# Kernel optimization log

Hardware: AMD Instinct MI355X
Metric: run time of the kernel (lower is better)

## Reference

```python
import jax, jax.numpy as jnp
import numpy as np

D_MODEL = 1024
N_HEAD = 16


def setup_inputs() -> dict:
    key = jax.random.key(0)
    ks = jax.random.split(key, 11)
    B, S, D = 2, 2048, D_MODEL
    scale = 1.0 / np.sqrt(D)
    inp = {
        "q": jax.random.normal(ks[0], (B, S, D), jnp.float32),
        "k": jax.random.normal(ks[1], (B, S, D), jnp.float32),
        "v": jax.random.normal(ks[2], (B, S, D), jnp.float32),
        "w_q": jax.random.normal(ks[3], (D, D), jnp.float32) * scale,
        "b_q": jnp.zeros((D,), jnp.float32),
        "w_k": jax.random.normal(ks[4], (D, D), jnp.float32) * scale,
        "b_k": jnp.zeros((D,), jnp.float32),
        "w_v": jax.random.normal(ks[5], (D, D), jnp.float32) * scale,
        "b_v": jnp.zeros((D,), jnp.float32),
        "w_o": jax.random.normal(ks[6], (D, D), jnp.float32) * scale,
        "b_o": jnp.zeros((D,), jnp.float32),
    }
    return inp


def _split_heads(x, n_head):
    # [B, S, D] -> [B, H, S, Dh]
    B, S, D = x.shape
    return x.reshape(B, S, n_head, D // n_head).transpose(0, 2, 1, 3)


def reference(q, k, v, w_q, b_q, w_k, b_k, w_v, b_v, w_o, b_o):
    # torch Linear: y = x @ W.T + b
    qp = q @ w_q.T + b_q
    kp = k @ w_k.T + b_k
    vp = v @ w_v.T + b_v
    qh = _split_heads(qp, N_HEAD)  # [B,H,S,Dh]
    kh = _split_heads(kp, N_HEAD)
    vh = _split_heads(vp, N_HEAD)
    d_head = qh.shape[-1]
    score = jnp.einsum("bhsd,bhtd->bhst", qh, kh) / jnp.sqrt(jnp.float32(d_head))
    attn = jax.nn.softmax(score, axis=-1)
    out = jnp.einsum("bhst,bhtd->bhsd", attn, vh)  # [B,H,S,Dh]
    B, H, S, Dh = out.shape
    out = out.transpose(0, 2, 1, 3).reshape(B, S, H * Dh)  # concat heads
    return out @ w_o.T + b_o
```

## Files before the change

kernel.cpp:

```cpp
#include <hip/hip_runtime.h>

typedef __bf16 bf16_t;
typedef __bf16 bf16x8 __attribute__((ext_vector_type(8)));
typedef __bf16 bf16x4 __attribute__((ext_vector_type(4)));
typedef float f32x4 __attribute__((ext_vector_type(4)));

#define MFMA16(a, b, c) __builtin_amdgcn_mfma_f32_16x16x32_bf16((a), (b), (c), 0, 0, 0)

#define GLOAD_LDS16(gsrc, ldst)                                                     \
  __builtin_amdgcn_global_load_lds(                                                 \
      (const __attribute__((address_space(1))) void*)(gsrc),                        \
      (__attribute__((address_space(3))) void*)(ldst), 16, 0, 0)

__global__ __launch_bounds__(256) void cast_all(
    const float* __restrict__ s0, const float* __restrict__ s1, const float* __restrict__ s2,
    const float* __restrict__ s3, const float* __restrict__ s4, const float* __restrict__ s5,
    const float* __restrict__ s6,
    bf16_t* __restrict__ d0, bf16_t* __restrict__ d1, bf16_t* __restrict__ d2,
    bf16_t* __restrict__ d3, bf16_t* __restrict__ d4, bf16_t* __restrict__ d5,
    bf16_t* __restrict__ d6) {
  const int a = blockIdx.y;
  const float* s = a == 0 ? s0 : a == 1 ? s1 : a == 2 ? s2 : a == 3 ? s3
                 : a == 4 ? s4 : a == 5 ? s5 : s6;
  bf16_t* d = a == 0 ? d0 : a == 1 ? d1 : a == 2 ? d2 : a == 3 ? d3
            : a == 4 ? d4 : a == 5 ? d5 : d6;
  const int n = a < 3 ? (2 * 2048 * 1024) : (1024 * 1024);
  int i = (blockIdx.x * 256 + threadIdx.x) * 4;
  if (i >= n) return;
  float4 v = *reinterpret_cast<const float4*>(s + i);
  bf16x4 o;
  o[0] = (bf16_t)v.x; o[1] = (bf16_t)v.y; o[2] = (bf16_t)v.z; o[3] = (bf16_t)v.w;
  *reinterpret_cast<bf16x4*>(d + i) = o;
}

template <int OUTF32>
__device__ __forceinline__ void gemm_core(
    const bf16_t* __restrict__ A, const bf16_t* __restrict__ B,
    const float* __restrict__ bias, void* __restrict__ Cout,
    int bm, int bn, float scalep, bf16_t* __restrict__ As, bf16_t* __restrict__ Bs) {
  const int tid = threadIdx.x, lane = tid & 63, wid = tid >> 6;
  const int wr = wid >> 1, wc = wid & 1;
  const int l15 = lane & 15, g = lane >> 4, l7 = l15 & 7;
  const int sr = lane >> 3;
  const int sg = (lane & 7) ^ sr;
  f32x4 acc[4][2] = {};

  const bf16_t* Arow = A + (size_t)(bm + wid * 32 + sr) * 1024 + sg * 8;
  const bf16_t* Brow = B + (size_t)(bn + wid * 16 + sr) * 1024 + sg * 8;

  auto stage = [&](int t, int buf) {
    const int k0 = t * 64;
    bf16_t* Ad = As + buf * 8192 + wid * 2048;
    bf16_t* Bd = Bs + buf * 4096 + wid * 1024;
#pragma unroll
    for (int a = 0; a < 4; a++)
      GLOAD_LDS16(Arow + (size_t)a * 8 * 1024 + k0, Ad + a * 512);
#pragma unroll
    for (int bI = 0; bI < 2; bI++)
      GLOAD_LDS16(Brow + (size_t)bI * 8 * 1024 + k0, Bd + bI * 512);
  };

  stage(0, 0);
  __syncthreads();
  for (int t = 0; t < 16; t++) {
    if (t < 15) stage(t + 1, (t + 1) & 1);
    const bf16_t* Ab = As + (t & 1) * 8192;
    const bf16_t* Bb = Bs + (t & 1) * 4096;
#pragma unroll
    for (int kk = 0; kk < 2; kk++) {
      const int gsw = ((kk * 4 + g) ^ l7) * 8;
      bf16x8 af[4], bfr[2];
#pragma unroll
      for (int mi = 0; mi < 4; mi++)
        af[mi] = *reinterpret_cast<const bf16x8*>(&Ab[(wr * 64 + mi * 16 + l15) * 64 + gsw]);
#pragma unroll
      for (int ni = 0; ni < 2; ni++)
        bfr[ni] = *reinterpret_cast<const bf16x8*>(&Bb[(wc * 32 + ni * 16 + l15) * 64 + gsw]);
      __builtin_amdgcn_s_setprio(1);
#pragma unroll
      for (int mi = 0; mi < 4; mi++)
#pragma unroll
        for (int ni = 0; ni < 2; ni++)
          acc[mi][ni] = MFMA16(af[mi], bfr[ni], acc[mi][ni]);
      __builtin_amdgcn_s_setprio(0);
    }
    __syncthreads();
  }

#pragma unroll
  for (int mi = 0; mi < 4; mi++)
#pragma unroll
    for (int ni = 0; ni < 2; ni++) {
      const int row = bm + wr * 64 + mi * 16 + g * 4;
      const int col = bn + wc * 32 + ni * 16 + l15;
      const float bv = bias[col];
#pragma unroll
      for (int r = 0; r < 4; r++) {
        float v = (acc[mi][ni][r] + bv) * scalep;
        if (OUTF32)
          reinterpret_cast<float*>(Cout)[(size_t)(row + r) * 1024 + col] = v;
        else
          reinterpret_cast<bf16_t*>(Cout)[(size_t)(row + r) * 1024 + col] = (bf16_t)v;
      }
    }
}

__global__ __launch_bounds__(256) void qkv_gemm(
    const bf16_t* __restrict__ qb, const bf16_t* __restrict__ kb, const bf16_t* __restrict__ vb,
    const bf16_t* __restrict__ wqb, const bf16_t* __restrict__ wkb, const bf16_t* __restrict__ wvb,
    const float* __restrict__ bq, const float* __restrict__ bk, const float* __restrict__ bv,
    bf16_t* __restrict__ QP, bf16_t* __restrict__ KP, bf16_t* __restrict__ VP, float qscale) {
  __shared__ bf16_t As[2 * 128 * 64];
  __shared__ bf16_t Bs[2 * 64 * 64];
  const int id = blockIdx.x;
  const int sw = (id & 7) * 192 + (id >> 3);
  const int z = sw >> 9, rem = sw & 511;
  const int by = rem >> 4, bx = rem & 15;
  const bf16_t* A = z == 0 ? qb : z == 1 ? kb : vb;
  const bf16_t* B = z == 0 ? wqb : z == 1 ? wkb : wvb;
  const float* bias = z == 0 ? bq : z == 1 ? bk : bv;
  bf16_t* C = z == 0 ? QP : z == 1 ? KP : VP;
  gemm_core<0>(A, B, bias, C, by * 128, bx * 64, z == 0 ? qscale : 1.0f, As, Bs);
}

__global__ __launch_bounds__(256) void out_gemm(
    const bf16_t* __restrict__ A, const bf16_t* __restrict__ B,
    const float* __restrict__ bias, float* __restrict__ C) {
  __shared__ bf16_t As[2 * 128 * 64];
  __shared__ bf16_t Bs[2 * 64 * 64];
  const int id = blockIdx.x;
  const int sw = (id & 7) * 64 + (id >> 3);
  const int by = sw >> 4, bx = sw & 15;
  gemm_core<1>(A, B, bias, C, by * 128, bx * 64, 1.0f, As, Bs);
}

__global__ __launch_bounds__(256) void transpose_v64(
    const bf16_t* __restrict__ VP, bf16_t* __restrict__ VT) {
  __shared__ bf16_t t[64][72];
  const int tid = threadIdx.x;
  const int bh = blockIdx.y, b = bh >> 4, h = bh & 15;
  const int sbase = blockIdx.x * 64;
#pragma unroll
  for (int i = 0; i < 2; i++) {
    int c = tid + i * 256;
    int r = c >> 3, cc = (c & 7) * 8;
    *reinterpret_cast<bf16x8*>(&t[r][cc]) =
        *reinterpret_cast<const bf16x8*>(&VP[(size_t)(b * 2048 + sbase + r) * 1024 + h * 64 + cc]);
  }
  __syncthreads();
#pragma unroll
  for (int i = 0; i < 2; i++) {
    int c = tid + i * 256;
    int d = c >> 3, scc = (c & 7) * 8;
    bf16x8 v;
#pragma unroll
    for (int j = 0; j < 8; j++) v[j] = t[scc + j][d];
    *reinterpret_cast<bf16x8*>(&VT[(size_t)(bh * 64 + d) * 2048 + sbase + scc]) = v;
  }
}

__global__ __launch_bounds__(512) void attn_fwd(
    const bf16_t* __restrict__ Q, const bf16_t* __restrict__ K,
    const bf16_t* __restrict__ VT, bf16_t* __restrict__ O) {
  __shared__ bf16_t Kl[2 * 64 * 64];
  __shared__ bf16_t Vl[2 * 64 * 64];
  __shared__ bf16_t Pl[8][16 * 64];
  const int tid = threadIdx.x, lane = tid & 63, wid = tid >> 6;
  const int l15 = lane & 15, g = lane >> 4, l7 = l15 & 7;
  const int id = blockIdx.x;
  const int sw = (id & 7) * 64 + (id >> 3);
  const int bh = sw >> 4, qblk = sw & 15;
  const int b = bh >> 4, h = bh & 15;
  const int qbase = qblk * 128;

  const int qrow = b * 2048 + qbase + wid * 16 + l15;
  const bf16x8 qf0 = *reinterpret_cast<const bf16x8*>(&Q[(size_t)qrow * 1024 + h * 64 + g * 8]);
  const bf16x8 qf1 = *reinterpret_cast<const bf16x8*>(&Q[(size_t)qrow * 1024 + h * 64 + 32 + g * 8]);

  const int sr = lane >> 3, sg = (lane & 7) ^ sr;
  const bf16_t* Ksrc = K + (size_t)(b * 2048 + wid * 8 + sr) * 1024 + h * 64 + sg * 8;
  const bf16_t* Vsrc = VT + (size_t)(bh * 64 + wid * 8 + sr) * 2048 + sg * 8;

  float ssum = 0.0f;
  f32x4 oacc[4] = {};

  auto stage = [&](int kt, int buf) {
    GLOAD_LDS16(Ksrc + (size_t)kt * 1024, Kl + buf * 4096 + wid * 512);
    GLOAD_LDS16(Vsrc + kt, Vl + buf * 4096 + wid * 512);
  };

  stage(0, 0);
  __syncthreads();
  for (int t = 0; t < 32; t++) {
    if (t < 31) stage((t + 1) * 64, (t + 1) & 1);
    const bf16_t* Kb = Kl + (t & 1) * 4096;
    const bf16_t* Vb = Vl + (t & 1) * 4096;

    f32x4 sacc[4] = {};
    __builtin_amdgcn_s_setprio(1);
#pragma unroll
    for (int ni = 0; ni < 4; ni++) {
      const int krow = (ni * 16 + l15) * 64;
      bf16x8 kf0 = *reinterpret_cast<const bf16x8*>(&Kb[krow + ((g ^ l7) * 8)]);
      bf16x8 kf1 = *reinterpret_cast<const bf16x8*>(&Kb[krow + (((4 + g) ^ l7) * 8)]);
      sacc[ni] = MFMA16(kf0, qf0, sacc[ni]);
      sacc[ni] = MFMA16(kf1, qf1, sacc[ni]);
    }
    __builtin_amdgcn_s_setprio(0);

    float rs = 0.0f;
#pragma unroll
    for (int ni = 0; ni < 4; ni++)
#pragma unroll
      for (int r = 0; r < 4; r++) {
        float e = exp2f(sacc[ni][r]);
        sacc[ni][r] = e;
        rs += e;
      }
    rs += __shfl_xor(rs, 16);
    rs += __shfl_xor(rs, 32);
    ssum += rs;

#pragma unroll
    for (int ni = 0; ni < 4; ni++) {
      bf16x4 pv;
#pragma unroll
      for (int r = 0; r < 4; r++) pv[r] = (bf16_t)sacc[ni][r];
      *reinterpret_cast<bf16x4*>(
          &Pl[wid][l15 * 64 + (((2 * ni + (g >> 1)) ^ l7) * 8) + (g & 1) * 4]) = pv;
    }

    __builtin_amdgcn_s_setprio(1);
#pragma unroll
    for (int c = 0; c < 2; c++) {
      const int gp = ((c * 4 + g) ^ l7) * 8;
      bf16x8 pf = *reinterpret_cast<const bf16x8*>(&Pl[wid][l15 * 64 + gp]);
#pragma unroll
      for (int dn = 0; dn < 4; dn++) {
        bf16x8 vf = *reinterpret_cast<const bf16x8*>(&Vb[(dn * 16 + l15) * 64 + gp]);
        oacc[dn] = MFMA16(pf, vf, oacc[dn]);
      }
    }
    __builtin_amdgcn_s_setprio(0);
    __syncthreads();
  }

  float si[4];
#pragma unroll
  for (int r = 0; r < 4; r++) si[r] = 1.0f / __shfl(ssum, g * 4 + r);
  const int orow = b * 2048 + qbase + wid * 16 + g * 4;
#pragma unroll
  for (int dn = 0; dn < 4; dn++)
#pragma unroll
    for (int r = 0; r < 4; r++)
      O[(size_t)(orow + r) * 1024 + h * 64 + dn * 16 + l15] = (bf16_t)(oacc[dn][r] * si[r]);
}

extern "C" void kernel_launch(void* const* d_in, const int* in_sizes, int n_in,
                              void* d_out, int out_size, void* d_ws, size_t ws_size,
                              hipStream_t stream) {
  const float* q  = (const float*)d_in[0];
  const float* k  = (const float*)d_in[1];
  const float* v  = (const float*)d_in[2];
  const float* wq = (const float*)d_in[3];
  const float* bq = (const float*)d_in[4];
  const float* wk = (const float*)d_in[5];
  const float* bk = (const float*)d_in[6];
  const float* wv = (const float*)d_in[7];
  const float* bv = (const float*)d_in[8];
  const float* wo = (const float*)d_in[9];
  const float* bo = (const float*)d_in[10];

  char* ws = (char*)d_ws;
  const size_t MB = 1024 * 1024;
  bf16_t* qb  = (bf16_t*)(ws + 0 * MB);
  bf16_t* kb  = (bf16_t*)(ws + 8 * MB);
  bf16_t* vb  = (bf16_t*)(ws + 16 * MB);
  bf16_t* QP  = (bf16_t*)(ws + 24 * MB);
  bf16_t* KP  = (bf16_t*)(ws + 32 * MB);
  bf16_t* VP  = (bf16_t*)(ws + 40 * MB);
  bf16_t* wqb = (bf16_t*)(ws + 48 * MB);
  bf16_t* wkb = (bf16_t*)(ws + 50 * MB);
  bf16_t* wvb = (bf16_t*)(ws + 52 * MB);
  bf16_t* wob = (bf16_t*)(ws + 54 * MB);
  bf16_t* VTb = (bf16_t*)(ws + 8 * MB);
  bf16_t* AO  = (bf16_t*)(ws + 0 * MB);

  const float QSCALE = 0.125f * 1.44269504089f;

  cast_all<<<dim3(4096, 7), 256, 0, stream>>>(q, k, v, wq, wk, wv, wo,
                                              qb, kb, vb, wqb, wkb, wvb, wob);
  qkv_gemm<<<1536, 256, 0, stream>>>(qb, kb, vb, wqb, wkb, wvb, bq, bk, bv,
                                     QP, KP, VP, QSCALE);
  transpose_v64<<<dim3(32, 32), 256, 0, stream>>>(VP, VTb);
  attn_fwd<<<512, 512, 0, stream>>>(QP, KP, VTb, AO);
  out_gemm<<<512, 256, 0, stream>>>(AO, wob, bo, (float*)d_out);
}
```

Baseline: 237.8 us.

## Enlarge GEMM tiles to 128x128 and move attention to 32x32 MFMA

The projection GEMMs switch from 128x64 tiles with K-step 64 to 128x128 tiles with K-step 32. That halves the grid and raises per-wave MFMA reuse, and an explicit vmcnt wait plus raw barriers replaces __syncthreads. The attention kernel drops to 256 threads with 32 query rows per wave and uses 32x32x16 MFMAs for both QK^T and PV, with matching P layout and normalisation via shared memory. The aim is fewer LDS reads per FLOP and less barrier overhead. The cost is more registers per wave and fewer blocks or waves to hide latency.

```diff
diff --git a/kernel.cpp b/kernel.cpp
--- a/kernel.cpp
+++ b/kernel.cpp
@@ -4,8 +4,10 @@
 typedef __bf16 bf16x8 __attribute__((ext_vector_type(8)));
 typedef __bf16 bf16x4 __attribute__((ext_vector_type(4)));
 typedef float f32x4 __attribute__((ext_vector_type(4)));
+typedef float f32x16 __attribute__((ext_vector_type(16)));
 
 #define MFMA16(a, b, c) __builtin_amdgcn_mfma_f32_16x16x32_bf16((a), (b), (c), 0, 0, 0)
+#define MFMA32(a, b, c) __builtin_amdgcn_mfma_f32_32x32x16_bf16((a), (b), (c), 0, 0, 0)
 
 #define GLOAD_LDS16(gsrc, ldst)                                                     \
   __builtin_amdgcn_global_load_lds(                                                 \
@@ -34,65 +36,65 @@
 }
 
 template <int OUTF32>
-__device__ __forceinline__ void gemm_core(
+__device__ __forceinline__ void gemm128(
     const bf16_t* __restrict__ A, const bf16_t* __restrict__ B,
     const float* __restrict__ bias, void* __restrict__ Cout,
     int bm, int bn, float scalep, bf16_t* __restrict__ As, bf16_t* __restrict__ Bs) {
   const int tid = threadIdx.x, lane = tid & 63, wid = tid >> 6;
   const int wr = wid >> 1, wc = wid & 1;
-  const int l15 = lane & 15, g = lane >> 4, l7 = l15 & 7;
-  const int sr = lane >> 3;
-  const int sg = (lane & 7) ^ sr;
-  f32x4 acc[4][2] = {};
-
-  const bf16_t* Arow = A + (size_t)(bm + wid * 32 + sr) * 1024 + sg * 8;
-  const bf16_t* Brow = B + (size_t)(bn + wid * 16 + sr) * 1024 + sg * 8;
-
-  auto stage = [&](int t, int buf) {
-    const int k0 = t * 64;
-    bf16_t* Ad = As + buf * 8192 + wid * 2048;
-    bf16_t* Bd = Bs + buf * 4096 + wid * 1024;
-#pragma unroll
-    for (int a = 0; a < 4; a++)
-      GLOAD_LDS16(Arow + (size_t)a * 8 * 1024 + k0, Ad + a * 512);
-#pragma unroll
-    for (int bI = 0; bI < 2; bI++)
-      GLOAD_LDS16(Brow + (size_t)bI * 8 * 1024 + k0, Bd + bI * 512);
+  const int l15 = lane & 15, g = lane >> 4;
+  f32x4 acc[4][4] = {};
+
+  const int srow0 = wid * 16 + (lane >> 2);
+  const int srow1 = 64 + wid * 16 + (lane >> 2);
+  const int sc = (lane & 3) * 8;
+  const bf16_t* Ap0 = A + (size_t)(bm + srow0) * 1024 + sc;
+  const bf16_t* Ap1 = A + (size_t)(bm + srow1) * 1024 + sc;
+  const bf16_t* Bp0 = B + (size_t)(bn + srow0) * 1024 + sc;
+  const bf16_t* Bp1 = B + (size_t)(bn + srow1) * 1024 + sc;
+
+  auto stage = [&](int k0, int buf) {
+    bf16_t* Ad = As + buf * 4096;
+    bf16_t* Bd = Bs + buf * 4096;
+    GLOAD_LDS16(Ap0 + k0, Ad + wid * 512);
+    GLOAD_LDS16(Ap1 + k0, Ad + 2048 + wid * 512);
+    GLOAD_LDS16(Bp0 + k0, Bd + wid * 512);
+    GLOAD_LDS16(Bp1 + k0, Bd + 2048 + wid * 512);
   };
 
   stage(0, 0);
-  __syncthreads();
-  for (int t = 0; t < 16; t++) {
-    if (t < 15) stage(t + 1, (t + 1) & 1);
-    const bf16_t* Ab = As + (t & 1) * 8192;
+  for (int t = 0; t < 32; t++) {
+    const int kn = (t < 31) ? (t + 1) * 32 : 0;
+    stage(kn, (t + 1) & 1);
+    asm volatile("s_waitcnt vmcnt(4)" ::: "memory");
+    __builtin_amdgcn_s_barrier();
+    __builtin_amdgcn_sched_barrier(0);
+    const bf16_t* Ab = As + (t & 1) * 4096;
     const bf16_t* Bb = Bs + (t & 1) * 4096;
-#pragma unroll
-    for (int kk = 0; kk < 2; kk++) {
-      const int gsw = ((kk * 4 + g) ^ l7) * 8;
-      bf16x8 af[4], bfr[2];
-#pragma unroll
-      for (int mi = 0; mi < 4; mi++)
-        af[mi] = *reinterpret_cast<const bf16x8*>(&Ab[(wr * 64 + mi * 16 + l15) * 64 + gsw]);
-#pragma unroll
-      for (int ni = 0; ni < 2; ni++)
-        bfr[ni] = *reinterpret_cast<const bf16x8*>(&Bb[(wc * 32 + ni * 16 + l15) * 64 + gsw]);
-      __builtin_amdgcn_s_setprio(1);
-#pragma unroll
-      for (int mi = 0; mi < 4; mi++)
-#pragma unroll
-        for (int ni = 0; ni < 2; ni++)
-          acc[mi][ni] = MFMA16(af[mi], bfr[ni], acc[mi][ni]);
-      __builtin_amdgcn_s_setprio(0);
-    }
-    __syncthreads();
+    bf16x8 af[4], bfr[4];
+#pragma unroll
+    for (int mi = 0; mi < 4; mi++)
+      af[mi] = *reinterpret_cast<const bf16x8*>(&Ab[(wr * 64 + mi * 16 + l15) * 32 + g * 8]);
+#pragma unroll
+    for (int ni = 0; ni < 4; ni++)
+      bfr[ni] = *reinterpret_cast<const bf16x8*>(&Bb[(wc * 64 + ni * 16 + l15) * 32 + g * 8]);
+    __builtin_amdgcn_s_setprio(1);
+#pragma unroll
+    for (int mi = 0; mi < 4; mi++)
+#pragma unroll
+      for (int ni = 0; ni < 4; ni++)
+        acc[mi][ni] = MFMA16(af[mi], bfr[ni], acc[mi][ni]);
+    __builtin_amdgcn_s_setprio(0);
+    __builtin_amdgcn_sched_barrier(0);
+    __builtin_amdgcn_s_barrier();
   }
 
 #pragma unroll
   for (int mi = 0; mi < 4; mi++)
 #pragma unroll
-    for (int ni = 0; ni < 2; ni++) {
+    for (int ni = 0; ni < 4; ni++) {
       const int row = bm + wr * 64 + mi * 16 + g * 4;
-      const int col = bn + wc * 32 + ni * 16 + l15;
+      const int col = bn + wc * 64 + ni * 16 + l15;
       const float bv = bias[col];
 #pragma unroll
       for (int r = 0; r < 4; r++) {
@@ -110,28 +112,28 @@
     const bf16_t* __restrict__ wqb, const bf16_t* __restrict__ wkb, const bf16_t* __restrict__ wvb,
     const float* __restrict__ bq, const float* __restrict__ bk, const float* __restrict__ bv,
     bf16_t* __restrict__ QP, bf16_t* __restrict__ KP, bf16_t* __restrict__ VP, float qscale) {
-  __shared__ bf16_t As[2 * 128 * 64];
-  __shared__ bf16_t Bs[2 * 64 * 64];
+  __shared__ bf16_t As[2 * 4096];
+  __shared__ bf16_t Bs[2 * 4096];
   const int id = blockIdx.x;
-  const int sw = (id & 7) * 192 + (id >> 3);
-  const int z = sw >> 9, rem = sw & 511;
-  const int by = rem >> 4, bx = rem & 15;
+  const int sw = (id & 7) * 96 + (id >> 3);
+  const int z = sw >> 8, rem = sw & 255;
+  const int by = rem >> 3, bx = rem & 7;
   const bf16_t* A = z == 0 ? qb : z == 1 ? kb : vb;
   const bf16_t* B = z == 0 ? wqb : z == 1 ? wkb : wvb;
   const float* bias = z == 0 ? bq : z == 1 ? bk : bv;
   bf16_t* C = z == 0 ? QP : z == 1 ? KP : VP;
-  gemm_core<0>(A, B, bias, C, by * 128, bx * 64, z == 0 ? qscale : 1.0f, As, Bs);
+  gemm128<0>(A, B, bias, C, by * 128, bx * 128, z == 0 ? qscale : 1.0f, As, Bs);
 }
 
 __global__ __launch_bounds__(256) void out_gemm(
     const bf16_t* __restrict__ A, const bf16_t* __restrict__ B,
     const float* __restrict__ bias, float* __restrict__ C) {
-  __shared__ bf16_t As[2 * 128 * 64];
-  __shared__ bf16_t Bs[2 * 64 * 64];
+  __shared__ bf16_t As[2 * 4096];
+  __shared__ bf16_t Bs[2 * 4096];
   const int id = blockIdx.x;
-  const int sw = (id & 7) * 64 + (id >> 3);
-  const int by = sw >> 4, bx = sw & 15;
-  gemm_core<1>(A, B, bias, C, by * 128, bx * 64, 1.0f, As, Bs);
+  const int sw = (id & 7) * 32 + (id >> 3);
+  const int by = sw >> 3, bx = sw & 7;
+  gemm128<1>(A, B, bias, C, by * 128, bx * 128, 1.0f, As, Bs);
 }
 
 __global__ __launch_bounds__(256) void transpose_v64(
@@ -159,101 +161,122 @@
   }
 }
 
-__global__ __launch_bounds__(512) void attn_fwd(
+__global__ __launch_bounds__(256) void attn_fwd(
     const bf16_t* __restrict__ Q, const bf16_t* __restrict__ K,
     const bf16_t* __restrict__ VT, bf16_t* __restrict__ O) {
-  __shared__ bf16_t Kl[2 * 64 * 64];
-  __shared__ bf16_t Vl[2 * 64 * 64];
-  __shared__ bf16_t Pl[8][16 * 64];
+  __shared__ bf16_t Kl[2 * 4096];
+  __shared__ bf16_t Vl[2 * 4096];
+  __shared__ bf16_t Pl[4][2048];
+  __shared__ float Sl[4][32];
   const int tid = threadIdx.x, lane = tid & 63, wid = tid >> 6;
-  const int l15 = lane & 15, g = lane >> 4, l7 = l15 & 7;
+  const int l31 = lane & 31, hsel = lane >> 5, l7 = lane & 7;
   const int id = blockIdx.x;
   const int sw = (id & 7) * 64 + (id >> 3);
   const int bh = sw >> 4, qblk = sw & 15;
   const int b = bh >> 4, h = bh & 15;
   const int qbase = qblk * 128;
 
-  const int qrow = b * 2048 + qbase + wid * 16 + l15;
-  const bf16x8 qf0 = *reinterpret_cast<const bf16x8*>(&Q[(size_t)qrow * 1024 + h * 64 + g * 8]);
-  const bf16x8 qf1 = *reinterpret_cast<const bf16x8*>(&Q[(size_t)qrow * 1024 + h * 64 + 32 + g * 8]);
-
-  const int sr = lane >> 3, sg = (lane & 7) ^ sr;
-  const bf16_t* Ksrc = K + (size_t)(b * 2048 + wid * 8 + sr) * 1024 + h * 64 + sg * 8;
-  const bf16_t* Vsrc = VT + (size_t)(bh * 64 + wid * 8 + sr) * 2048 + sg * 8;
+  const int qrow = b * 2048 + qbase + wid * 32 + l31;
+  bf16x8 qf[4];
+#pragma unroll
+  for (int ks = 0; ks < 4; ks++)
+    qf[ks] = *reinterpret_cast<const bf16x8*>(
+        &Q[(size_t)qrow * 1024 + h * 64 + ks * 16 + hsel * 8]);
+
+  const int srow = lane >> 3;
+  const int sg = (lane & 7) ^ srow;
+  const bf16_t* Ksrc = K + (size_t)(b * 2048 + wid * 16 + srow) * 1024 + h * 64 + sg * 8;
+  const bf16_t* Vsrc = VT + (size_t)(bh * 64 + wid * 16 + srow) * 2048 + sg * 8;
+
+  auto stage = [&](int kt, int buf) {
+    bf16_t* Kd = Kl + buf * 4096 + wid * 1024;
+    bf16_t* Vd = Vl + buf * 4096 + wid * 1024;
+    GLOAD_LDS16(Ksrc + (size_t)kt * 1024, Kd);
+    GLOAD_LDS16(Ksrc + (size_t)(kt + 8) * 1024, Kd + 512);
+    GLOAD_LDS16(Vsrc + kt, Vd);
+    GLOAD_LDS16(Vsrc + kt + 8 * 2048, Vd + 512);
+  };
 
   float ssum = 0.0f;
-  f32x4 oacc[4] = {};
-
-  auto stage = [&](int kt, int buf) {
-    GLOAD_LDS16(Ksrc + (size_t)kt * 1024, Kl + buf * 4096 + wid * 512);
-    GLOAD_LDS16(Vsrc + kt, Vl + buf * 4096 + wid * 512);
-  };
+  f32x16 oacc[2] = {};
 
   stage(0, 0);
-  __syncthreads();
   for (int t = 0; t < 32; t++) {
-    if (t < 31) stage((t + 1) * 64, (t + 1) & 1);
+    const int ktn = (t < 31) ? (t + 1) * 64 : 0;
+    stage(ktn, (t + 1) & 1);
+    asm volatile("s_waitcnt vmcnt(4)" ::: "memory");
+    __builtin_amdgcn_s_barrier();
+    __builtin_amdgcn_sched_barrier(0);
     const bf16_t* Kb = Kl + (t & 1) * 4096;
     const bf16_t* Vb = Vl + (t & 1) * 4096;
 
-    f32x4 sacc[4] = {};
+    f32x16 sacc[2] = {};
     __builtin_amdgcn_s_setprio(1);
 #pragma unroll
-    for (int ni = 0; ni < 4; ni++) {
-      const int krow = (ni * 16 + l15) * 64;
-      bf16x8 kf0 = *reinterpret_cast<const bf16x8*>(&Kb[krow + ((g ^ l7) * 8)]);
-      bf16x8 kf1 = *reinterpret_cast<const bf16x8*>(&Kb[krow + (((4 + g) ^ l7) * 8)]);
-      sacc[ni] = MFMA16(kf0, qf0, sacc[ni]);
-      sacc[ni] = MFMA16(kf1, qf1, sacc[ni]);
-    }
+    for (int ni = 0; ni < 2; ni++)
+#pragma unroll
+      for (int ks = 0; ks < 4; ks++) {
+        bf16x8 kf = *reinterpret_cast<const bf16x8*>(
+            &Kb[(ni * 32 + l31) * 64 + ((2 * ks + hsel) ^ l7) * 8]);
+        sacc[ni] = MFMA32(kf, qf[ks], sacc[ni]);
+      }
     __builtin_amdgcn_s_setprio(0);
 
     float rs = 0.0f;
 #pragma unroll
-    for (int ni = 0; ni < 4; ni++)
-#pragma unroll
-      for (int r = 0; r < 4; r++) {
+    for (int ni = 0; ni < 2; ni++)
+#pragma unroll
+      for (int r = 0; r < 16; r++) {
         float e = exp2f(sacc[ni][r]);
         sacc[ni][r] = e;
         rs += e;
       }
-    rs += __shfl_xor(rs, 16);
     rs += __shfl_xor(rs, 32);
     ssum += rs;
 
 #pragma unroll
-    for (int ni = 0; ni < 4; ni++) {
-      bf16x4 pv;
-#pragma unroll
-      for (int r = 0; r < 4; r++) pv[r] = (bf16_t)sacc[ni][r];
-      *reinterpret_cast<bf16x4*>(
-          &Pl[wid][l15 * 64 + (((2 * ni + (g >> 1)) ^ l7) * 8) + (g & 1) * 4]) = pv;
-    }
+    for (int ni = 0; ni < 2; ni++)
+#pragma unroll
+      for (int a = 0; a < 4; a++) {
+        bf16x4 pv;
+#pragma unroll
+        for (int r = 0; r < 4; r++) pv[r] = (bf16_t)sacc[ni][a * 4 + r];
+        *reinterpret_cast<bf16x4*>(
+            &Pl[wid][l31 * 64 + (((a + 4 * ni) ^ l7) * 8) + hsel * 4]) = pv;
+      }
 
     __builtin_amdgcn_s_setprio(1);
 #pragma unroll
-    for (int c = 0; c < 2; c++) {
-      const int gp = ((c * 4 + g) ^ l7) * 8;
-      bf16x8 pf = *reinterpret_cast<const bf16x8*>(&Pl[wid][l15 * 64 + gp]);
-#pragma unroll
-      for (int dn = 0; dn < 4; dn++) {
-        bf16x8 vf = *reinterpret_cast<const bf16x8*>(&Vb[(dn * 16 + l15) * 64 + gp]);
-        oacc[dn] = MFMA16(pf, vf, oacc[dn]);
+    for (int ks = 0; ks < 4; ks++) {
+      bf16x8 pf = *reinterpret_cast<const bf16x8*>(
+          &Pl[wid][l31 * 64 + ((2 * ks + hsel) ^ l7) * 8]);
+#pragma unroll
+      for (int dI = 0; dI < 2; dI++) {
+        bf16x8 vf = *reinterpret_cast<const bf16x8*>(
+            &Vb[(dI * 32 + l31) * 64 + ((2 * ks + hsel) ^ l7) * 8]);
+        oacc[dI] = MFMA32(pf, vf, oacc[dI]);
       }
     }
     __builtin_amdgcn_s_setprio(0);
-    __syncthreads();
-  }
-
-  float si[4];
-#pragma unroll
-  for (int r = 0; r < 4; r++) si[r] = 1.0f / __shfl(ssum, g * 4 + r);
-  const int orow = b * 2048 + qbase + wid * 16 + g * 4;
-#pragma unroll
-  for (int dn = 0; dn < 4; dn++)
-#pragma unroll
-    for (int r = 0; r < 4; r++)
-      O[(size_t)(orow + r) * 1024 + h * 64 + dn * 16 + l15] = (bf16_t)(oacc[dn][r] * si[r]);
+    __builtin_amdgcn_sched_barrier(0);
+    __builtin_amdgcn_s_barrier();
+  }
+
+  if (lane < 32) Sl[wid][l31] = 1.0f / ssum;
+  __builtin_amdgcn_s_barrier();
+  const int qg = b * 2048 + qbase + wid * 32;
+#pragma unroll
+  for (int a = 0; a < 4; a++) {
+    f32x4 siv = *reinterpret_cast<const f32x4*>(&Sl[wid][a * 8 + hsel * 4]);
+#pragma unroll
+    for (int rr = 0; rr < 4; rr++) {
+      const int row = qg + a * 8 + hsel * 4 + rr;
+#pragma unroll
+      for (int dI = 0; dI < 2; dI++)
+        O[(size_t)row * 1024 + h * 64 + dI * 32 + l31] =
+            (bf16_t)(oacc[dI][a * 4 + rr] * siv[rr]);
+    }
+  }
 }
 
 extern "C" void kernel_launch(void* const* d_in, const int* in_sizes, int n_in,
@@ -290,9 +313,9 @@
 
   cast_all<<<dim3(4096, 7), 256, 0, stream>>>(q, k, v, wq, wk, wv, wo,
                                               qb, kb, vb, wqb, wkb, wvb, wob);
-  qkv_gemm<<<1536, 256, 0, stream>>>(qb, kb, vb, wqb, wkb, wvb, bq, bk, bv,
-                                     QP, KP, VP, QSCALE);
+  qkv_gemm<<<768, 256, 0, stream>>>(qb, kb, vb, wqb, wkb, wvb, bq, bk, bv,
+                                    QP, KP, VP, QSCALE);
   transpose_v64<<<dim3(32, 32), 256, 0, stream>>>(VP, VTb);
-  attn_fwd<<<512, 512, 0, stream>>>(QP, KP, VTb, AO);
-  out_gemm<<<512, 256, 0, stream>>>(AO, wob, bo, (float*)d_out);
-}
+  attn_fwd<<<512, 256, 0, stream>>>(QP, KP, VTb, AO);
+  out_gemm<<<256, 256, 0, stream>>>(AO, wob, bo, (float*)d_out);
+}
```

Result: slower. 251.8 us (+5.9%).
